# Optimization experiments

Hardware: AMD Instinct MI355X
Metric: run time of the kernel (lower is better)

The kernel has to match this reference:

```python
import jax, jax.numpy as jnp
from jax import lax
import numpy as np

V, D, L, E = 32000, 256, 4, 4
B, S = 1, 4096  # B must be 1: AstroNorm's buffer update/broadcast only works for batch==1
SIG = float(1.0 / (1.0 + np.exp(-0.15)))        # sigmoid(init_sparsity=0.15), static (int() detaches)
K_GATE = max(1, int(S * SIG))                    # tokens kept by sparsity gate
K_EXP = max(1, int(0.8 * E))                     # int(sparsity_constraint * num_experts) = 3


def setup_inputs() -> dict:
    key = jax.random.key(0)
    ks = jax.random.split(key, 8)
    s = 0.02
    return {
        "tokens": jax.random.randint(ks[0], (B, S), 0, V),
        "emb": jax.random.normal(ks[1], (V, D)) * s,
        "buffers": jax.random.normal(ks[2], (L, D)) * 0.1,   # AstroNorm buffer per layer
        "decays": jnp.full((L,), 0.95),                       # AstroNorm decay per layer
        "gate_w": jax.random.normal(ks[3], (L, D)) * s,       # context_gate (Linear(dim,1,bias=False))
        "gating_W": jax.random.normal(ks[4], (L, E, D)) * s,  # expert router
        "gating_b": jnp.zeros((L, E)),
        "exp_W": jax.random.normal(ks[5], (L, E, D, D)) * s,  # per-expert Linear(dim,dim)
        "exp_b": jnp.zeros((L, E, D)),
        "ln_g": jnp.ones((D,)),
        "ln_b": jnp.zeros((D,)),
        "head_W": jax.random.normal(ks[6], (V, D)) * s,
        "head_b": jnp.zeros((V,)),
    }


def _forward(tokens, emb, buffers, decays, gate_w, gating_W, gating_b,
             exp_W, exp_b, ln_g, ln_b, head_W, head_b):
    x = emb[tokens]  # [B,S,D]
    for l in range(L):
        # ---- AstroNorm: stats over sequence dim (dim=1), detached as in torch ----
        mu = lax.stop_gradient(jnp.mean(x, axis=1, keepdims=True))           # [B,1,D]
        var = lax.stop_gradient(jnp.var(x, axis=1, keepdims=True, ddof=1))   # unbiased var
        new_buf = decays[l] * buffers[l] + (1.0 - decays[l]) * mu.squeeze()  # [D] (B==1)
        x = jnp.where(jnp.abs(x - mu) > jnp.abs(new_buf), mu, x) / jnp.sqrt(var + 1e-6)
        # ---- DynamicSparsityGate: keep tokens strictly above k-th score ----
        scores = jnp.einsum('bsd,d->bs', x, gate_w[l])
        thr = lax.top_k(scores, K_GATE)[0][:, -1:]           # k-th largest per row
        x = x * (scores > thr).astype(x.dtype)[..., None]
        # ---- SparseExpert: top-K_EXP experts per token, masked accumulation ----
        gs = jnp.einsum('bsd,ed->bse', x, gating_W[l]) + gating_b[l]
        idx = lax.top_k(gs, K_EXP)[1]                                    # [B,S,k]
        emask = (jax.nn.one_hot(idx, E).sum(-2) > 0).astype(x.dtype)     # [B,S,E]
        ys = jnp.einsum('bsd,eod->bseo', x, exp_W[l]) + exp_b[l]         # all-expert outputs
        x = jnp.einsum('bse,bseo->bso', emask, ys)
    # ---- LayerNorm (biased var, eps=1e-5) + vocab head ----
    mu = jnp.mean(x, axis=-1, keepdims=True)
    v = jnp.var(x, axis=-1, keepdims=True)
    x = (x - mu) / jnp.sqrt(v + 1e-5) * ln_g + ln_b
    return jnp.einsum('bsd,vd->bsv', x, head_W) + head_b


def reference(tokens, emb, buffers, decays, gate_w, gating_W, gating_b,
              exp_W, exp_b, ln_g, ln_b, head_W, head_b):
    return _forward(tokens, emb, buffers, decays, gate_w, gating_W, gating_b,
                    exp_W, exp_b, ln_g, ln_b, head_W, head_b)
```

## Files before the change

### kernel.cpp

```cpp
#include <hip/hip_runtime.h>
#include <hip/hip_bf16.h>
#include <math.h>

#define V 32000
#define D 256
#define L 4
#define E 4
#define S 4096
#define K_GATE 2201
#define NCH 64
#define SCHUNK 64
#define CTS 136


typedef __hip_bfloat16 bf16;
typedef __attribute__((ext_vector_type(8))) short bf16x8;
typedef __attribute__((ext_vector_type(4))) float f32x4;

__device__ __forceinline__ float loadf(const void* p, size_t i, int bf) {
    if (bf) return __bfloat162float(((const bf16*)p)[i]);
    return ((const float*)p)[i];
}
__device__ __forceinline__ float us2f(unsigned short u) {
    return __uint_as_float((unsigned)u << 16);
}

#define GLDS16(g, l)                                                            \
    __builtin_amdgcn_global_load_lds(                                           \
        (const __attribute__((address_space(1))) unsigned int*)(g),             \
        (__attribute__((address_space(3))) unsigned int*)(l), 16, 0, 0)

__device__ __forceinline__ void stage_tile(const bf16* __restrict__ src, int rowStride,
                                           short* lds, int t, int k0) {
    int w = t >> 6, l = t & 63;
    #pragma unroll
    for (int i = 0; i < 2; i++) {
        int chunk = (w * 2 + i) * 64 + l;
        int row = chunk >> 2;
        int c8 = (chunk & 3) ^ ((row >> 1) & 3);
        const bf16* g = src + (size_t)row * rowStride + k0 + c8 * 8;
        GLDS16(g, (char*)lds + (size_t)(w * 2 + i) * 1024);
    }
}

__device__ __forceinline__ bf16x8 frag_ld(const short* lds, int row, int quad) {
    return *(const bf16x8*)&lds[row * 32 + ((quad ^ ((row >> 1) & 3)) << 3)];
}

__global__ void k_detect(const void* __restrict__ emb, int* __restrict__ flag) {
    const unsigned short* h = (const unsigned short*)emb;
    int cnt = 0;
    for (int i = 0; i < 128; i += 2) {
        int e = (h[i] >> 7) & 0xFF;
        if (e >= 100 && e <= 130) cnt++;
    }
    *flag = (cnt >= 32) ? 1 : 0;
}

__global__ void k_wcast(const void* __restrict__ W, const int* __restrict__ bfp,
                        bf16* __restrict__ Wb) {
    if (*bfp) return;
    size_t idx = ((size_t)blockIdx.x * 256 + threadIdx.x) * 4;
    float4 v = *(const float4*)((const float*)W + idx);
    Wb[idx + 0] = __float2bfloat16(v.x);
    Wb[idx + 1] = __float2bfloat16(v.y);
    Wb[idx + 2] = __float2bfloat16(v.z);
    Wb[idx + 3] = __float2bfloat16(v.w);
}

__global__ void k_embed(const int* __restrict__ tok, const void* __restrict__ emb,
                        const int* __restrict__ bfp, float* __restrict__ x) {
    int s = blockIdx.x, d = threadIdx.x;
    int bf = *bfp;
    int t = tok[s];
    x[s * D + d] = loadf(emb, (size_t)t * D + d, bf);
}

__global__ void k_stats_part(const float* __restrict__ x, float* __restrict__ psum,
                             float* __restrict__ psq) {
    int b = blockIdx.x;
    int t = threadIdx.x;
    float s = 0.f, q = 0.f;
    int s0 = b * SCHUNK;
    #pragma unroll 4
    for (int i = 0; i < SCHUNK; i++) {
        float v = x[(size_t)(s0 + i) * D + t];
        s += v; q += v * v;
    }
    psum[b * D + t] = s;
    psq[b * D + t] = q;
}

__global__ void k_norm_score(float* __restrict__ x, const float* __restrict__ psum,
                             const float* __restrict__ psq,
                             const void* __restrict__ buffers, const void* __restrict__ decays,
                             const void* __restrict__ gate_w, const int* __restrict__ bfp,
                             int l, float* __restrict__ scores) {
    __shared__ float mu_s[D], rstd_s[D], absnb_s[D];
    int t = threadIdx.x, w = t >> 6, ln = t & 63;
    int bf = *bfp;
    {
        float s = 0.f, q = 0.f;
        #pragma unroll 8
        for (int b = 0; b < NCH; b++) { s += psum[b * D + t]; q += psq[b * D + t]; }
        float m = s / (float)S;
        float var = (q - (float)S * m * m) / (float)(S - 1);
        float dec = loadf(decays, l, bf);
        float nb = dec * loadf(buffers, l * D + t, bf) + (1.f - dec) * m;
        mu_s[t] = m;
        rstd_s[t] = rsqrtf(var + 1e-6f);
        absnb_s[t] = fabsf(nb);
    }
    __syncthreads();
    int s = blockIdx.x * 4 + w;
    float part = 0.f;
    #pragma unroll
    for (int j = 0; j < 4; j++) {
        int f = ln + j * 64;
        float m = mu_s[f];
        float v = x[(size_t)s * D + f];
        float xv = (fabsf(v - m) > absnb_s[f]) ? m : v;
        xv *= rstd_s[f];
        x[(size_t)s * D + f] = xv;
        part += xv * loadf(gate_w, l * D + f, bf);
    }
    #pragma unroll
    for (int m2 = 1; m2 < 64; m2 <<= 1) part += __shfl_xor(part, m2, 64);
    if (ln == 0) scores[s] = part;
}

__global__ void k_thr(const float* __restrict__ scores, float* __restrict__ thr) {
    __shared__ unsigned keys[S];
    __shared__ unsigned hist[256];
    __shared__ unsigned sh_pref, sh_rank, sh_bucket;
    int t = threadIdx.x;
    #pragma unroll
    for (int i = 0; i < 4; i++) {
        int idx = i * 1024 + t;
        unsigned u = __float_as_uint(scores[idx]);
        keys[idx] = (u & 0x80000000u) ? ~u : (u | 0x80000000u);
    }
    if (t == 0) { sh_pref = 0u; sh_rank = S - K_GATE; }
    __syncthreads();
    for (int shift = 24; shift >= 0; shift -= 8) {
        if (t < 256) hist[t] = 0u;
        __syncthreads();
        unsigned pref = sh_pref, r = sh_rank;
        unsigned pmask = (shift == 24) ? 0u : (0xFFFFFFFFu << (shift + 8));
        #pragma unroll
        for (int i = 0; i < 4; i++) {
            unsigned k = keys[i * 1024 + t];
            if ((k & pmask) == pref) atomicAdd(&hist[(k >> shift) & 0xFF], 1u);
        }
        __syncthreads();
        if (t < 64) {
            unsigned h[4];
            unsigned loc = 0u;
            #pragma unroll
            for (int j = 0; j < 4; j++) { h[j] = hist[t * 4 + j]; loc += h[j]; }
            unsigned pre = loc;
            #pragma unroll
            for (int off = 1; off < 64; off <<= 1) {
                unsigned u2 = __shfl_up(pre, off, 64);
                if (t >= off) pre += u2;
            }
            unsigned base = pre - loc;
            if (r >= base && r < pre) {
                unsigned rr = r - base;
                int bsel = -1;
                #pragma unroll
                for (int j = 0; j < 4; j++) {
                    if (bsel < 0) {
                        if (rr < h[j]) bsel = j;
                        else rr -= h[j];
                    }
                }
                sh_bucket = (unsigned)(t * 4 + bsel);
                sh_rank = rr;
            }
        }
        __syncthreads();
        if (t == 0) sh_pref = pref | (sh_bucket << shift);
        __syncthreads();
    }
    if (t == 0) {
        unsigned k = sh_pref;
        unsigned u = (k & 0x80000000u) ? (k ^ 0x80000000u) : ~k;
        thr[0] = __uint_as_float(u);
    }
}

__global__ void k_route(const float* __restrict__ x, const float* __restrict__ scores,
                        const float* __restrict__ thr,
                        const void* __restrict__ gating_W, const void* __restrict__ gating_b,
                        const int* __restrict__ bfp, int l, int* __restrict__ excl) {
    int t = threadIdx.x, w = t >> 6, ln = t & 63;
    int s = blockIdx.x * 4 + w;
    int bf = *bfp;
    float keep = (scores[s] > thr[0]) ? 1.f : 0.f;
    float xv[4];
    #pragma unroll
    for (int j = 0; j < 4; j++)
        xv[j] = x[(size_t)s * D + ln + j * 64] * keep;
    float gs[E];
    #pragma unroll
    for (int e = 0; e < E; e++) {
        float p = 0.f;
        #pragma unroll
        for (int j = 0; j < 4; j++)
            p += xv[j] * loadf(gating_W, (size_t)(l * E + e) * D + ln + j * 64, bf);
        #pragma unroll
        for (int m2 = 1; m2 < 64; m2 <<= 1) p += __shfl_xor(p, m2, 64);
        gs[e] = p + loadf(gating_b, l * E + e, bf);
    }
    if (ln == 0) {
        int mi = 0;
        float mv = gs[0];
        #pragma unroll
        for (int e = 1; e < E; e++) if (gs[e] <= mv) { mv = gs[e]; mi = e; }
        excl[s] = mi;
    }
}

#define MBM 32
#define MBN 64
#define MBK 32
__global__ __launch_bounds__(256) void k_moe(const float* __restrict__ x,
                                             const float* __restrict__ scores,
                                             const float* __restrict__ thr,
                                             const int* __restrict__ excl,
                                             const void* __restrict__ exp_W,
                                             const void* __restrict__ exp_b,
                                             const int* __restrict__ bfp, int l,
                                             float* __restrict__ xo) {
    __shared__ float As[MBK][MBM + 2];
    __shared__ float Bs[E][MBK][MBN + 4];
    __shared__ float kp[MBM];
    __shared__ int exs[MBM];
    int bf = *bfp;
    int bnf = blockIdx.x * MBN;
    int bm = blockIdx.y * MBM;
    int t = threadIdx.x;
    int tm = (t >> 4) * 2;
    int tn = (t & 15) * 4;
    if (t < MBM) {
        kp[t] = (scores[bm + t] > thr[0]) ? 1.f : 0.f;
        exs[t] = excl[bm + t];
    }
    __syncthreads();
    const unsigned short* Wb16 = (const unsigned short*)exp_W;
    const float* Wf32 = (const float*)exp_W;
    size_t wbase = (size_t)l * E * D * D;
    float acc[E][2][4] = {};
    for (int k0 = 0; k0 < D; k0 += MBK) {
        {
            int m = t >> 3, c4 = t & 7;
            float4 v = *(const float4*)&x[(size_t)(bm + m) * D + k0 + c4 * 4];
            float kk = kp[m];
            As[c4 * 4 + 0][m] = v.x * kk;
            As[c4 * 4 + 1][m] = v.y * kk;
            As[c4 * 4 + 2][m] = v.z * kk;
            As[c4 * 4 + 3][m] = v.w * kk;
        }
        int n = t >> 2, c8 = t & 3;
        #pragma unroll
        for (int e = 0; e < E; e++) {
            size_t roff = wbase + ((size_t)e * D + bnf + n) * D + k0 + c8 * 8;
            if (bf) {
                ushort4 v0 = *(const ushort4*)(Wb16 + roff);
                ushort4 v1 = *(const ushort4*)(Wb16 + roff + 4);
                Bs[e][c8 * 8 + 0][n] = us2f(v0.x);
                Bs[e][c8 * 8 + 1][n] = us2f(v0.y);
                Bs[e][c8 * 8 + 2][n] = us2f(v0.z);
                Bs[e][c8 * 8 + 3][n] = us2f(v0.w);
                Bs[e][c8 * 8 + 4][n] = us2f(v1.x);
                Bs[e][c8 * 8 + 5][n] = us2f(v1.y);
                Bs[e][c8 * 8 + 6][n] = us2f(v1.z);
                Bs[e][c8 * 8 + 7][n] = us2f(v1.w);
            } else {
                float4 v0 = *(const float4*)(Wf32 + roff);
                float4 v1 = *(const float4*)(Wf32 + roff + 4);
                Bs[e][c8 * 8 + 0][n] = v0.x;
                Bs[e][c8 * 8 + 1][n] = v0.y;
                Bs[e][c8 * 8 + 2][n] = v0.z;
                Bs[e][c8 * 8 + 3][n] = v0.w;
                Bs[e][c8 * 8 + 4][n] = v1.x;
                Bs[e][c8 * 8 + 5][n] = v1.y;
                Bs[e][c8 * 8 + 6][n] = v1.z;
                Bs[e][c8 * 8 + 7][n] = v1.w;
            }
        }
        __syncthreads();
        #pragma unroll 4
        for (int k = 0; k < MBK; k++) {
            float a0 = As[k][tm];
            float a1 = As[k][tm + 1];
            #pragma unroll
            for (int e = 0; e < E; e++) {
                float4 b = *(const float4*)&Bs[e][k][tn];
                acc[e][0][0] += a0 * b.x;
                acc[e][0][1] += a0 * b.y;
                acc[e][0][2] += a0 * b.z;
                acc[e][0][3] += a0 * b.w;
                acc[e][1][0] += a1 * b.x;
                acc[e][1][1] += a1 * b.y;
                acc[e][1][2] += a1 * b.z;
                acc[e][1][3] += a1 * b.w;
            }
        }
        __syncthreads();
    }
    float fin[2][4] = {};
    #pragma unroll
    for (int e = 0; e < E; e++) {
        float be[4];
        #pragma unroll
        for (int j = 0; j < 4; j++)
            be[j] = loadf(exp_b, (size_t)(l * E + e) * D + bnf + tn + j, bf);
        #pragma unroll
        for (int i = 0; i < 2; i++) {
            if (exs[tm + i] != e) {
                #pragma unroll
                for (int j = 0; j < 4; j++)
                    fin[i][j] += acc[e][i][j] + be[j];
            }
        }
    }
    #pragma unroll
    for (int i = 0; i < 2; i++) {
        float4 o = { fin[i][0], fin[i][1], fin[i][2], fin[i][3] };
        *(float4*)&xo[(size_t)(bm + tm + i) * D + bnf + tn] = o;
    }
}

__global__ void k_ln(const float* __restrict__ x, const void* __restrict__ g,
                     const void* __restrict__ b, const int* __restrict__ bfp,
                     bf16* __restrict__ xnb) {
    int t = threadIdx.x, w = t >> 6, ln = t & 63;
    int s = blockIdx.x * 4 + w;
    int bf = *bfp;
    float vv[4];
    float sum = 0.f, sq = 0.f;
    #pragma unroll
    for (int j = 0; j < 4; j++) {
        float v = x[(size_t)s * D + ln + j * 64];
        vv[j] = v; sum += v; sq += v * v;
    }
    #pragma unroll
    for (int m2 = 1; m2 < 64; m2 <<= 1) {
        sum += __shfl_xor(sum, m2, 64);
        sq  += __shfl_xor(sq, m2, 64);
    }
    float m = sum / (float)D;
    float var = sq / (float)D - m * m;
    float r = rsqrtf(var + 1e-5f);
    #pragma unroll
    for (int j = 0; j < 4; j++) {
        int f = ln + j * 64;
        xnb[(size_t)s * D + f] = __float2bfloat16((vv[j] - m) * r * loadf(g, f, bf)
                                                  + loadf(b, f, bf));
    }
}

__global__ __launch_bounds__(256) void k_head_mfma(const bf16* __restrict__ xnb,
                                                   const void* __restrict__ head_W_raw,
                                                   const bf16* __restrict__ Wb,
                                                   const void* __restrict__ bias,
                                                   const int* __restrict__ bfp,
                                                   void* __restrict__ out) {
    __shared__ __align__(16) char smem[128 * CTS * 2];
    short* At = (short*)smem;
    short* Bt = (short*)(smem + 8192);
    short* Ct = (short*)smem;
    int bf = *bfp;
    const bf16* Wsrc = bf ? (const bf16*)head_W_raw : Wb;
    int bs = blockIdx.x * 128;
    int bv = blockIdx.y * 128;
    int t = threadIdx.x;
    int wave = t >> 6, lane = t & 63;
    int wm = (wave >> 1) * 64, wn = (wave & 1) * 64;
    int quad = lane >> 4, l16 = lane & 15;

    f32x4 acc[4][4] = {};
    for (int k0 = 0; k0 < D; k0 += 32) {
        stage_tile(xnb + (size_t)bs * D, D, At, t, k0);
        stage_tile(Wsrc + (size_t)bv * D, D, Bt, t, k0);
        __syncthreads();
        bf16x8 af[4], bfg[4];
        #pragma unroll
        for (int i = 0; i < 4; i++) af[i]  = frag_ld(At, wm + i * 16 + l16, quad);
        #pragma unroll
        for (int j = 0; j < 4; j++) bfg[j] = frag_ld(Bt, wn + j * 16 + l16, quad);
        #pragma unroll
        for (int i = 0; i < 4; i++)
            #pragma unroll
            for (int j = 0; j < 4; j++)
                acc[i][j] = __builtin_amdgcn_mfma_f32_16x16x32_bf16(af[i], bfg[j], acc[i][j], 0, 0, 0);
        __syncthreads();
    }
    if (bf) {
        #pragma unroll
        for (int j = 0; j < 4; j++) {
            int colL = wn + j * 16 + l16;
            float bb = __bfloat162float(((const bf16*)bias)[bv + colL]);
            #pragma unroll
            for (int i = 0; i < 4; i++) {
                int rowL = wm + i * 16 + quad * 4;
                #pragma unroll
                for (int rg = 0; rg < 4; rg++) {
                    bf16 hv = __float2bfloat16(acc[i][j][rg] + bb);
                    Ct[(rowL + rg) * CTS + colL] = *(short*)&hv;
                }
            }
        }
        __syncthreads();
        bf16* ob = (bf16*)out;
        #pragma unroll
        for (int k = 0; k < 8; k++) {
            int cc = k * 256 + t;
            int row = cc >> 4, c16 = cc & 15;
            bf16x8 v = *(const bf16x8*)&Ct[row * CTS + c16 * 8];
            *(bf16x8*)(ob + (size_t)(bs + row) * V + bv + c16 * 8) = v;
        }
    } else {
        float* of = (float*)out;
        #pragma unroll
        for (int j = 0; j < 4; j++) {
            int col = bv + wn + j * 16 + l16;
            float bb = loadf(bias, col, bf);
            #pragma unroll
            for (int i = 0; i < 4; i++) {
                int row0 = bs + wm + i * 16 + quad * 4;
                #pragma unroll
                for (int rg = 0; rg < 4; rg++)
                    of[(size_t)(row0 + rg) * V + col] = acc[i][j][rg] + bb;
            }
        }
    }
}

extern "C" void kernel_launch(void* const* d_in, const int* in_sizes, int n_in,
                              void* d_out, int out_size, void* d_ws, size_t ws_size,
                              hipStream_t stream) {
    const int*  tokens   = (const int*)d_in[0];
    const void* emb      = d_in[1];
    const void* buffers  = d_in[2];
    const void* decays   = d_in[3];
    const void* gate_w   = d_in[4];
    const void* gating_W = d_in[5];
    const void* gating_b = d_in[6];
    const void* exp_W    = d_in[7];
    const void* exp_b    = d_in[8];
    const void* ln_g     = d_in[9];
    const void* ln_b     = d_in[10];
    const void* head_W   = d_in[11];
    const void* head_b   = d_in[12];

    char* p = (char*)d_ws;
    bf16* Wb    = (bf16*)p;             p += (size_t)V * D * 2;
    bf16* xnb   = (bf16*)p;             p += (size_t)S * D * 2;
    float* xA   = (float*)p;            p += (size_t)S * D * 4;
    float* xB   = (float*)p;            p += (size_t)S * D * 4;
    float* psum = (float*)p;            p += (size_t)NCH * D * 4;
    float* psq  = (float*)p;            p += (size_t)NCH * D * 4;
    float* scores = (float*)p;          p += (size_t)S * 4;
    int* excl   = (int*)p;              p += (size_t)S * 4;
    float* thr  = (float*)p;            p += 16;
    int* flag   = (int*)p;              p += 16;

    k_detect<<<1, 1, 0, stream>>>(emb, flag);
    k_wcast<<<(V * D) / 1024, 256, 0, stream>>>(head_W, flag, Wb);
    k_embed<<<S, D, 0, stream>>>(tokens, emb, flag, xA);

    float* xc = xA;
    float* xo = xB;
    for (int l = 0; l < L; l++) {
        k_stats_part<<<NCH, 256, 0, stream>>>(xc, psum, psq);
        k_norm_score<<<S / 4, 256, 0, stream>>>(xc, psum, psq, buffers, decays,
                                                gate_w, flag, l, scores);
        k_thr<<<1, 1024, 0, stream>>>(scores, thr);
        k_route<<<S / 4, 256, 0, stream>>>(xc, scores, thr, gating_W, gating_b,
                                           flag, l, excl);
        dim3 gm(D / MBN, S / MBM);
        k_moe<<<gm, 256, 0, stream>>>(xc, scores, thr, excl, exp_W, exp_b, flag, l, xo);
        float* tmp = xc; xc = xo; xo = tmp;
    }
    k_ln<<<S / 4, 256, 0, stream>>>(xc, ln_g, ln_b, flag, xnb);
    dim3 gh(S / 128, V / 128);
    k_head_mfma<<<gh, 256, 0, stream>>>(xnb, head_W, Wb, head_b, flag, d_out);
}
```

Baseline: 989.8 us.

## Enlarge MoE per-thread register tile and swizzle head GEMM block order

The MoE expert GEMM now runs with 128 threads per block, and each thread computes a 4x4 output tile per expert instead of 2x4. A-tile reads become a float4 shared-memory load, and the staging loops are reorganised so the smaller block still fills the tiles. This raises arithmetic per shared-memory load but adds accumulator registers (64 floats) and halves the threads per block. Separately, the vocab-head GEMM remaps block IDs with an XCD-style swizzle so consecutive blocks on the same chiplet share head_W tiles in cache.

```diff
diff --git a/kernel.cpp b/kernel.cpp
--- a/kernel.cpp
+++ b/kernel.cpp
@@ -225,7 +225,7 @@
 #define MBM 32
 #define MBN 64
 #define MBK 32
-__global__ __launch_bounds__(256) void k_moe(const float* __restrict__ x,
+__global__ __launch_bounds__(128) void k_moe(const float* __restrict__ x,
                                              const float* __restrict__ scores,
                                              const float* __restrict__ thr,
                                              const int* __restrict__ excl,
@@ -233,7 +233,7 @@
                                              const void* __restrict__ exp_b,
                                              const int* __restrict__ bfp, int l,
                                              float* __restrict__ xo) {
-    __shared__ float As[MBK][MBM + 2];
+    __shared__ float As[MBK][MBM + 4];
     __shared__ float Bs[E][MBK][MBN + 4];
     __shared__ float kp[MBM];
     __shared__ int exs[MBM];
@@ -241,7 +241,7 @@
     int bnf = blockIdx.x * MBN;
     int bm = blockIdx.y * MBM;
     int t = threadIdx.x;
-    int tm = (t >> 4) * 2;
+    int tm = (t >> 4) * 4;
     int tn = (t & 15) * 4;
     if (t < MBM) {
         kp[t] = (scores[bm + t] > thr[0]) ? 1.f : 0.f;
@@ -251,66 +251,74 @@
     const unsigned short* Wb16 = (const unsigned short*)exp_W;
     const float* Wf32 = (const float*)exp_W;
     size_t wbase = (size_t)l * E * D * D;
-    float acc[E][2][4] = {};
+    float acc[E][4][4] = {};
     for (int k0 = 0; k0 < D; k0 += MBK) {
         {
-            int m = t >> 3, c4 = t & 7;
-            float4 v = *(const float4*)&x[(size_t)(bm + m) * D + k0 + c4 * 4];
+            int m = t >> 2, c8 = t & 3;
             float kk = kp[m];
-            As[c4 * 4 + 0][m] = v.x * kk;
-            As[c4 * 4 + 1][m] = v.y * kk;
-            As[c4 * 4 + 2][m] = v.z * kk;
-            As[c4 * 4 + 3][m] = v.w * kk;
-        }
-        int n = t >> 2, c8 = t & 3;
-        #pragma unroll
-        for (int e = 0; e < E; e++) {
-            size_t roff = wbase + ((size_t)e * D + bnf + n) * D + k0 + c8 * 8;
-            if (bf) {
-                ushort4 v0 = *(const ushort4*)(Wb16 + roff);
-                ushort4 v1 = *(const ushort4*)(Wb16 + roff + 4);
-                Bs[e][c8 * 8 + 0][n] = us2f(v0.x);
-                Bs[e][c8 * 8 + 1][n] = us2f(v0.y);
-                Bs[e][c8 * 8 + 2][n] = us2f(v0.z);
-                Bs[e][c8 * 8 + 3][n] = us2f(v0.w);
-                Bs[e][c8 * 8 + 4][n] = us2f(v1.x);
-                Bs[e][c8 * 8 + 5][n] = us2f(v1.y);
-                Bs[e][c8 * 8 + 6][n] = us2f(v1.z);
-                Bs[e][c8 * 8 + 7][n] = us2f(v1.w);
-            } else {
-                float4 v0 = *(const float4*)(Wf32 + roff);
-                float4 v1 = *(const float4*)(Wf32 + roff + 4);
-                Bs[e][c8 * 8 + 0][n] = v0.x;
-                Bs[e][c8 * 8 + 1][n] = v0.y;
-                Bs[e][c8 * 8 + 2][n] = v0.z;
-                Bs[e][c8 * 8 + 3][n] = v0.w;
-                Bs[e][c8 * 8 + 4][n] = v1.x;
-                Bs[e][c8 * 8 + 5][n] = v1.y;
-                Bs[e][c8 * 8 + 6][n] = v1.z;
-                Bs[e][c8 * 8 + 7][n] = v1.w;
+            #pragma unroll
+            for (int h = 0; h < 2; h++) {
+                float4 v = *(const float4*)&x[(size_t)(bm + m) * D + k0 + c8 * 8 + h * 4];
+                As[c8 * 8 + h * 4 + 0][m] = v.x * kk;
+                As[c8 * 8 + h * 4 + 1][m] = v.y * kk;
+                As[c8 * 8 + h * 4 + 2][m] = v.z * kk;
+                As[c8 * 8 + h * 4 + 3][m] = v.w * kk;
+            }
+        }
+        {
+            int n = t >> 1, kb = (t & 1) * 16;
+            #pragma unroll
+            for (int e = 0; e < E; e++) {
+                size_t roff = wbase + ((size_t)e * D + bnf + n) * D + k0 + kb;
+                if (bf) {
+                    #pragma unroll
+                    for (int h = 0; h < 4; h++) {
+                        ushort4 v = *(const ushort4*)(Wb16 + roff + h * 4);
+                        Bs[e][kb + h * 4 + 0][n] = us2f(v.x);
+                        Bs[e][kb + h * 4 + 1][n] = us2f(v.y);
+                        Bs[e][kb + h * 4 + 2][n] = us2f(v.z);
+                        Bs[e][kb + h * 4 + 3][n] = us2f(v.w);
+                    }
+                } else {
+                    #pragma unroll
+                    for (int h = 0; h < 4; h++) {
+                        float4 v = *(const float4*)(Wf32 + roff + h * 4);
+                        Bs[e][kb + h * 4 + 0][n] = v.x;
+                        Bs[e][kb + h * 4 + 1][n] = v.y;
+                        Bs[e][kb + h * 4 + 2][n] = v.z;
+                        Bs[e][kb + h * 4 + 3][n] = v.w;
+                    }
+                }
             }
         }
         __syncthreads();
         #pragma unroll 4
         for (int k = 0; k < MBK; k++) {
-            float a0 = As[k][tm];
-            float a1 = As[k][tm + 1];
+            float4 a = *(const float4*)&As[k][tm];
             #pragma unroll
             for (int e = 0; e < E; e++) {
                 float4 b = *(const float4*)&Bs[e][k][tn];
-                acc[e][0][0] += a0 * b.x;
-                acc[e][0][1] += a0 * b.y;
-                acc[e][0][2] += a0 * b.z;
-                acc[e][0][3] += a0 * b.w;
-                acc[e][1][0] += a1 * b.x;
-                acc[e][1][1] += a1 * b.y;
-                acc[e][1][2] += a1 * b.z;
-                acc[e][1][3] += a1 * b.w;
-            }
-        }
-        __syncthreads();
-    }
-    float fin[2][4] = {};
+                acc[e][0][0] += a.x * b.x;
+                acc[e][0][1] += a.x * b.y;
+                acc[e][0][2] += a.x * b.z;
+                acc[e][0][3] += a.x * b.w;
+                acc[e][1][0] += a.y * b.x;
+                acc[e][1][1] += a.y * b.y;
+                acc[e][1][2] += a.y * b.z;
+                acc[e][1][3] += a.y * b.w;
+                acc[e][2][0] += a.z * b.x;
+                acc[e][2][1] += a.z * b.y;
+                acc[e][2][2] += a.z * b.z;
+                acc[e][2][3] += a.z * b.w;
+                acc[e][3][0] += a.w * b.x;
+                acc[e][3][1] += a.w * b.y;
+                acc[e][3][2] += a.w * b.z;
+                acc[e][3][3] += a.w * b.w;
+            }
+        }
+        __syncthreads();
+    }
+    float fin[4][4] = {};
     #pragma unroll
     for (int e = 0; e < E; e++) {
         float be[4];
@@ -318,7 +326,7 @@
         for (int j = 0; j < 4; j++)
             be[j] = loadf(exp_b, (size_t)(l * E + e) * D + bnf + tn + j, bf);
         #pragma unroll
-        for (int i = 0; i < 2; i++) {
+        for (int i = 0; i < 4; i++) {
             if (exs[tm + i] != e) {
                 #pragma unroll
                 for (int j = 0; j < 4; j++)
@@ -327,7 +335,7 @@
         }
     }
     #pragma unroll
-    for (int i = 0; i < 2; i++) {
+    for (int i = 0; i < 4; i++) {
         float4 o = { fin[i][0], fin[i][1], fin[i][2], fin[i][3] };
         *(float4*)&xo[(size_t)(bm + tm + i) * D + bnf + tn] = o;
     }
@@ -374,8 +382,10 @@
     short* Ct = (short*)smem;
     int bf = *bfp;
     const bf16* Wsrc = bf ? (const bf16*)head_W_raw : Wb;
-    int bs = blockIdx.x * 128;
-    int bv = blockIdx.y * 128;
+    int id = blockIdx.y * 32 + blockIdx.x;
+    int sw = (id & 7) * 1000 + (id >> 3);
+    int bs = (sw & 31) * 128;
+    int bv = (sw >> 5) * 128;
     int t = threadIdx.x;
     int wave = t >> 6, lane = t & 63;
     int wm = (wave >> 1) * 64, wn = (wave & 1) * 64;
@@ -482,7 +492,7 @@
         k_route<<<S / 4, 256, 0, stream>>>(xc, scores, thr, gating_W, gating_b,
                                            flag, l, excl);
         dim3 gm(D / MBN, S / MBM);
-        k_moe<<<gm, 256, 0, stream>>>(xc, scores, thr, excl, exp_W, exp_b, flag, l, xo);
+        k_moe<<<gm, 128, 0, stream>>>(xc, scores, thr, excl, exp_W, exp_b, flag, l, xo);
         float* tmp = xc; xc = xo; xo = tmp;
     }
     k_ln<<<S / 4, 256, 0, stream>>>(xc, ln_g, ln_b, flag, xnb);
```

Result: slower. 1.045 ms (+5.6%).
